# Optimization experiments

Measured on AMD Instinct MI355X. Metric: run time of the kernel, lower is better.

The kernel has to match this reference:

```python
import jax, jax.numpy as jnp
import numpy as np

N_NODES = 50000
N_EDGES = 500000
D_IN = 128
D_HID = 128
OUTPUT_DIM = 10.0


def gcn_conv(x, src, dst, edge_weight, W, b, n_nodes):
    # PyG GCNConv: out = D^{-1/2} (A + I) D^{-1/2} X W + b, self-loop weight 1
    xw = x @ W  # [N, D_out]
    # degree at target nodes, including self-loop weight 1
    deg = jax.ops.segment_sum(edge_weight, dst, num_segments=n_nodes) + 1.0
    dinv = jnp.where(deg > 0, jax.lax.rsqrt(deg), 0.0)  # [N]
    norm = dinv[src] * edge_weight * dinv[dst]  # [E]
    msgs = xw[src] * norm[:, None]  # [E, D_out] gathered+scaled messages
    agg = jax.ops.segment_sum(msgs, dst, num_segments=n_nodes)
    # analytic self-loop contribution: norm_ii = dinv_i * 1 * dinv_i
    agg = agg + xw * (dinv * dinv)[:, None]
    return agg + b


def setup_inputs() -> dict:
    key = jax.random.key(0)
    k = jax.random.split(key, 8)
    x = jax.random.normal(k[0], (N_NODES, D_IN), dtype=jnp.float32)
    edge_index = jax.random.randint(k[1], (2, N_EDGES), 0, N_NODES, dtype=jnp.int64)
    edge_weight = jax.random.uniform(k[2], (N_EDGES,), dtype=jnp.float32)
    s1 = 1.0 / np.sqrt(D_IN)
    s2 = 1.0 / np.sqrt(D_HID)
    W1 = jax.random.uniform(k[3], (D_IN, D_HID), minval=-s1, maxval=s1, dtype=jnp.float32)
    b1 = jnp.zeros((D_HID,), dtype=jnp.float32)
    W2 = jax.random.uniform(k[4], (D_HID, D_HID), minval=-s2, maxval=s2, dtype=jnp.float32)
    b2 = jnp.zeros((D_HID,), dtype=jnp.float32)
    Wf = jax.random.uniform(k[5], (D_HID, 1), minval=-s2, maxval=s2, dtype=jnp.float32)
    bf = jax.random.uniform(k[6], (1,), minval=-s2, maxval=s2, dtype=jnp.float32)
    return {"x": x, "edge_index": edge_index, "edge_weight": edge_weight,
            "W1": W1, "b1": b1, "W2": W2, "b2": b2, "Wf": Wf, "bf": bf}


def reference(x, edge_index, edge_weight, W1, b1, W2, b2, Wf, bf):
    src, dst = edge_index[0], edge_index[1]
    h = gcn_conv(x, src, dst, edge_weight, W1, b1, N_NODES)
    h = gcn_conv(h, src, dst, edge_weight, W2, b2, N_NODES)
    out = h @ Wf + bf  # [N, 1]
    return jax.nn.sigmoid(out) * OUTPUT_DIM
```

## Files before the change

kernel.cpp:

```cpp
#include <hip/hip_runtime.h>

#define N_NODES 50000
#define N_EDGES 500000
#define D 128
#define FXS 4194304.0f
#define CAP 64

typedef unsigned long long u64;

__global__ void pass1_kernel(const int* __restrict__ src, const int* __restrict__ dst,
                             const float* __restrict__ ew,
                             const float* __restrict__ W1, const float* __restrict__ W2,
                             const float* __restrict__ b1, const float* __restrict__ b2,
                             const float* __restrict__ Wf, const float* __restrict__ bf,
                             u64* __restrict__ degcnt, int2* __restrict__ pairs,
                             float* __restrict__ v, float* __restrict__ consts,
                             int eb) {
    if ((int)blockIdx.x == eb) {
        __shared__ float u[D];
        int t = threadIdx.x;
        if (t < D) {
            float a = 0.f;
#pragma unroll 8
            for (int j = 0; j < D; ++j) a += W2[t * D + j] * Wf[j];
            u[t] = a;
        }
        __syncthreads();
        if (t < D) {
            float a = 0.f;
#pragma unroll 8
            for (int k = 0; k < D; ++k) a += W1[t * D + k] * u[k];
            v[t] = a;
        }
        if (t == 0) {
            float c = 0.f;
            for (int k = 0; k < D; ++k) c += b1[k] * u[k];
            consts[0] = c;
        } else if (t == 1) {
            float c = bf[0];
            for (int k = 0; k < D; ++k) c += b2[k] * Wf[k];
            consts[1] = c;
        }
        return;
    }
    int tid = blockIdx.x * blockDim.x + threadIdx.x;
    if (tid < N_EDGES / 4) {
        int4   d = ((const int4*)dst)[tid];
        int4   s = ((const int4*)src)[tid];
        float4 w = ((const float4*)ew)[tid];
        unsigned f0 = __float2uint_rn(w.x * FXS);
        unsigned f1 = __float2uint_rn(w.y * FXS);
        unsigned f2 = __float2uint_rn(w.z * FXS);
        unsigned f3 = __float2uint_rn(w.w * FXS);
        u64 o0 = atomicAdd(&degcnt[d.x], (1ull << 32) | (u64)f0);
        u64 o1 = atomicAdd(&degcnt[d.y], (1ull << 32) | (u64)f1);
        u64 o2 = atomicAdd(&degcnt[d.z], (1ull << 32) | (u64)f2);
        u64 o3 = atomicAdd(&degcnt[d.w], (1ull << 32) | (u64)f3);
        int s0 = (int)(o0 >> 32), s1 = (int)(o1 >> 32);
        int s2 = (int)(o2 >> 32), s3 = (int)(o3 >> 32);
        if (s0 < CAP) pairs[d.x * CAP + s0] = make_int2(s.x, __float_as_int(w.x));
        if (s1 < CAP) pairs[d.y * CAP + s1] = make_int2(s.y, __float_as_int(w.y));
        if (s2 < CAP) pairs[d.z * CAP + s2] = make_int2(s.z, __float_as_int(w.z));
        if (s3 < CAP) pairs[d.w * CAP + s3] = make_int2(s.w, __float_as_int(w.w));
    }
}

__global__ void gemv_kernel(const float* __restrict__ x, const float* __restrict__ v,
                            const u64* __restrict__ degcnt,
                            float* __restrict__ dinv, float* __restrict__ tw,
                            int* __restrict__ cntv) {
    __shared__ float vs[D];
    const int t = threadIdx.x;
    if (t < D) vs[t] = v[t];
    __syncthreads();
    const int l = t & 31;
    const int n = blockIdx.x * 8 + (t >> 5);
    float4 xv = ((const float4*)(x + (size_t)n * D))[l];
    float a = xv.x * vs[l * 4] + xv.y * vs[l * 4 + 1] +
              xv.z * vs[l * 4 + 2] + xv.w * vs[l * 4 + 3];
#pragma unroll
    for (int off = 16; off > 0; off >>= 1) a += __shfl_xor(a, off);
    if (l == 0) {
        u64 dc = degcnt[n];
        int c = (int)(dc >> 32);
        float deg = (float)(unsigned)(dc & 0xffffffffu) * (1.0f / FXS);
        float di = rsqrtf(deg + 1.0f);
        dinv[n] = di;
        cntv[n] = (c < CAP) ? c : CAP;
        tw[n] = di * a;
    }
}

__global__ void gather_s_kernel(const float* __restrict__ tw, const float* __restrict__ dinv,
                                const int* __restrict__ cntv, const int2* __restrict__ pairs,
                                const float* __restrict__ consts, float* __restrict__ sw) {
    int tid = threadIdx.x;
    int n = blockIdx.x * 64 + (tid >> 2);
    int l = tid & 3;
    if (n >= N_NODES) return;
    int cnt = cntv[n];
    const int4* row = (const int4*)(pairs + (size_t)n * CAP);
    float acc = 0.f;
    for (int c = l; 2 * c < cnt; c += 4) {
        int4 p = row[c];
        acc += __int_as_float(p.y) * tw[p.x];
        if (2 * c + 1 < cnt) acc += __int_as_float(p.w) * tw[p.z];
    }
    acc += __shfl_xor(acc, 1);
    acc += __shfl_xor(acc, 2);
    if (l == 0) {
        float di = dinv[n];
        float s = di * (acc + tw[n]) + consts[0];
        sw[n] = di * s;
    }
}

__global__ void gather_z_kernel(const float* __restrict__ sw, const float* __restrict__ dinv,
                                const int* __restrict__ cntv, const int2* __restrict__ pairs,
                                const float* __restrict__ consts, float* __restrict__ out) {
    int tid = threadIdx.x;
    int n = blockIdx.x * 64 + (tid >> 2);
    int l = tid & 3;
    if (n >= N_NODES) return;
    int cnt = cntv[n];
    const int4* row = (const int4*)(pairs + (size_t)n * CAP);
    float acc = 0.f;
    for (int c = l; 2 * c < cnt; c += 4) {
        int4 p = row[c];
        acc += __int_as_float(p.y) * sw[p.x];
        if (2 * c + 1 < cnt) acc += __int_as_float(p.w) * sw[p.z];
    }
    acc += __shfl_xor(acc, 1);
    acc += __shfl_xor(acc, 2);
    if (l == 0) {
        float di = dinv[n];
        float z = di * (acc + sw[n]) + consts[1];
        out[n] = 10.0f / (1.0f + expf(-z));
    }
}

extern "C" void kernel_launch(void* const* d_in, const int* in_sizes, int n_in,
                              void* d_out, int out_size, void* d_ws, size_t ws_size,
                              hipStream_t stream) {
    const float* x  = (const float*)d_in[0];
    const int*   ei = (const int*)d_in[1];
    const float* ew = (const float*)d_in[2];
    const float* W1 = (const float*)d_in[3];
    const float* b1 = (const float*)d_in[4];
    const float* W2 = (const float*)d_in[5];
    const float* b2 = (const float*)d_in[6];
    const float* Wf = (const float*)d_in[7];
    const float* bf = (const float*)d_in[8];
    const int* srcv = ei;
    const int* dstv = ei + N_EDGES;
    float* out = (float*)d_out;

    char* p = (char*)d_ws;
    auto alloc = [&](size_t bytes) { void* r = (void*)p; p += (bytes + 255) & ~(size_t)255; return r; };
    u64*   degcnt = (u64*)alloc((size_t)N_NODES * 8);
    float* dinv   = (float*)alloc(N_NODES * 4);
    int*   cntv   = (int*)alloc(N_NODES * 4);
    float* tw     = (float*)alloc(N_NODES * 4);
    float* sw     = (float*)alloc(N_NODES * 4);
    float* v      = (float*)alloc(D * 4);
    float* consts = (float*)alloc(2 * 4);
    int2*  pairs  = (int2*)alloc((size_t)N_NODES * CAP * 8);

    const int EB = (N_EDGES / 4 + 255) / 256;
    const int GB = (N_NODES + 63) / 64;

    hipMemsetAsync(degcnt, 0, (size_t)N_NODES * 8, stream);

    pass1_kernel<<<EB + 1, 256, 0, stream>>>(srcv, dstv, ew, W1, W2, b1, b2, Wf, bf,
                                             degcnt, pairs, v, consts, EB);

    gemv_kernel<<<N_NODES / 8, 256, 0, stream>>>(x, v, degcnt, dinv, tw, cntv);

    gather_s_kernel<<<GB, 256, 0, stream>>>(tw, dinv, cntv, pairs, consts, sw);
    gather_z_kernel<<<GB, 256, 0, stream>>>(sw, dinv, cntv, pairs, consts, out);
}
```

Before: 131.2 us.

## Replace global 64-bit atomic bucketing with LDS chunk histograms, scan, and placement

Edge bucketing by destination moves off global 64-bit atomics. It now uses three phases. A per-chunk histogram is built in shared memory with 8-bit packed counters, a per-node scan over chunks produces base offsets, and a placement pass uses LDS atomics to assign slots. Degrees are computed in the gemv kernel by summing the stored edge weights rather than by fixed-point atomic accumulation. The aim is to remove contended global atomics and the memset, at the cost of extra kernels, a 256x50000-byte histogram round trip, and the risk of 8-bit counter overflow for high-degree nodes within a chunk. Degree now also ignores edges beyond CAP.

```diff
diff --git a/kernel.cpp b/kernel.cpp
--- a/kernel.cpp
+++ b/kernel.cpp
@@ -3,20 +3,20 @@
 #define N_NODES 50000
 #define N_EDGES 500000
 #define D 128
-#define FXS 4194304.0f
 #define CAP 64
+#define NCHUNK 256
+#define EPC ((N_EDGES + NCHUNK - 1) / NCHUNK)
+#define NWORDS ((N_NODES + 3) / 4)
 
 typedef unsigned long long u64;
 
-__global__ void pass1_kernel(const int* __restrict__ src, const int* __restrict__ dst,
-                             const float* __restrict__ ew,
-                             const float* __restrict__ W1, const float* __restrict__ W2,
-                             const float* __restrict__ b1, const float* __restrict__ b2,
-                             const float* __restrict__ Wf, const float* __restrict__ bf,
-                             u64* __restrict__ degcnt, int2* __restrict__ pairs,
-                             float* __restrict__ v, float* __restrict__ consts,
-                             int eb) {
-    if ((int)blockIdx.x == eb) {
+__global__ void hist_kernel(const int* __restrict__ dst,
+                            const float* __restrict__ W1, const float* __restrict__ W2,
+                            const float* __restrict__ b1, const float* __restrict__ b2,
+                            const float* __restrict__ Wf, const float* __restrict__ bf,
+                            unsigned* __restrict__ hist32, float* __restrict__ v,
+                            float* __restrict__ consts) {
+    if ((int)blockIdx.x == NCHUNK) {
         __shared__ float u[D];
         int t = threadIdx.x;
         if (t < D) {
@@ -43,32 +43,60 @@
         }
         return;
     }
-    int tid = blockIdx.x * blockDim.x + threadIdx.x;
-    if (tid < N_EDGES / 4) {
-        int4   d = ((const int4*)dst)[tid];
-        int4   s = ((const int4*)src)[tid];
-        float4 w = ((const float4*)ew)[tid];
-        unsigned f0 = __float2uint_rn(w.x * FXS);
-        unsigned f1 = __float2uint_rn(w.y * FXS);
-        unsigned f2 = __float2uint_rn(w.z * FXS);
-        unsigned f3 = __float2uint_rn(w.w * FXS);
-        u64 o0 = atomicAdd(&degcnt[d.x], (1ull << 32) | (u64)f0);
-        u64 o1 = atomicAdd(&degcnt[d.y], (1ull << 32) | (u64)f1);
-        u64 o2 = atomicAdd(&degcnt[d.z], (1ull << 32) | (u64)f2);
-        u64 o3 = atomicAdd(&degcnt[d.w], (1ull << 32) | (u64)f3);
-        int s0 = (int)(o0 >> 32), s1 = (int)(o1 >> 32);
-        int s2 = (int)(o2 >> 32), s3 = (int)(o3 >> 32);
-        if (s0 < CAP) pairs[d.x * CAP + s0] = make_int2(s.x, __float_as_int(w.x));
-        if (s1 < CAP) pairs[d.y * CAP + s1] = make_int2(s.y, __float_as_int(w.y));
-        if (s2 < CAP) pairs[d.z * CAP + s2] = make_int2(s.z, __float_as_int(w.z));
-        if (s3 < CAP) pairs[d.w * CAP + s3] = make_int2(s.w, __float_as_int(w.w));
+    __shared__ unsigned lds[NWORDS];
+    const int t = threadIdx.x;
+    const int c = blockIdx.x;
+    for (int i = t; i < NWORDS; i += 256) lds[i] = 0u;
+    __syncthreads();
+    const int e0 = c * EPC;
+    const int e1 = (e0 + EPC < N_EDGES) ? e0 + EPC : N_EDGES;
+    for (int e = e0 + t; e < e1; e += 256) {
+        int d = dst[e];
+        atomicAdd(&lds[d >> 2], 1u << (8 * (d & 3)));
+    }
+    __syncthreads();
+    unsigned* outw = hist32 + (size_t)c * NWORDS;
+    for (int i = t; i < NWORDS; i += 256) outw[i] = lds[i];
+}
+
+__global__ void scan_kernel(const unsigned char* __restrict__ hist8,
+                            unsigned char* __restrict__ base8, int* __restrict__ cntv) {
+    int n = blockIdx.x * blockDim.x + threadIdx.x;
+    if (n >= N_NODES) return;
+    int run = 0;
+#pragma unroll 8
+    for (int c = 0; c < NCHUNK; ++c) {
+        int b = hist8[(size_t)c * (NWORDS * 4) + n];
+        base8[(size_t)c * (NWORDS * 4) + n] = (unsigned char)run;
+        run += b;
+    }
+    cntv[n] = (run < CAP) ? run : CAP;
+}
+
+__global__ void place_kernel(const int* __restrict__ src, const int* __restrict__ dst,
+                             const float* __restrict__ ew,
+                             const unsigned* __restrict__ base32, int2* __restrict__ pairs) {
+    __shared__ unsigned lds[NWORDS];
+    const int t = threadIdx.x;
+    const int c = blockIdx.x;
+    const unsigned* inw = base32 + (size_t)c * NWORDS;
+    for (int i = t; i < NWORDS; i += 256) lds[i] = inw[i];
+    __syncthreads();
+    const int e0 = c * EPC;
+    const int e1 = (e0 + EPC < N_EDGES) ? e0 + EPC : N_EDGES;
+    for (int e = e0 + t; e < e1; e += 256) {
+        int d = dst[e];
+        int sh = 8 * (d & 3);
+        unsigned old = atomicAdd(&lds[d >> 2], 1u << sh);
+        int slot = (int)((old >> sh) & 0xffu);
+        if (slot < CAP)
+            pairs[(size_t)d * CAP + slot] = make_int2(src[e], __float_as_int(ew[e]));
     }
 }
 
 __global__ void gemv_kernel(const float* __restrict__ x, const float* __restrict__ v,
-                            const u64* __restrict__ degcnt,
-                            float* __restrict__ dinv, float* __restrict__ tw,
-                            int* __restrict__ cntv) {
+                            const int2* __restrict__ pairs, const int* __restrict__ cntv,
+                            float* __restrict__ dinv, float* __restrict__ tw) {
     __shared__ float vs[D];
     const int t = threadIdx.x;
     if (t < D) vs[t] = v[t];
@@ -78,15 +106,18 @@
     float4 xv = ((const float4*)(x + (size_t)n * D))[l];
     float a = xv.x * vs[l * 4] + xv.y * vs[l * 4 + 1] +
               xv.z * vs[l * 4 + 2] + xv.w * vs[l * 4 + 3];
+    int cnt = cntv[n];
+    const int2* row = pairs + (size_t)n * CAP;
+    float wsum = 0.f;
+    for (int i = l; i < cnt; i += 32) wsum += __int_as_float(row[i].y);
 #pragma unroll
-    for (int off = 16; off > 0; off >>= 1) a += __shfl_xor(a, off);
+    for (int off = 16; off > 0; off >>= 1) {
+        a    += __shfl_xor(a, off);
+        wsum += __shfl_xor(wsum, off);
+    }
     if (l == 0) {
-        u64 dc = degcnt[n];
-        int c = (int)(dc >> 32);
-        float deg = (float)(unsigned)(dc & 0xffffffffu) * (1.0f / FXS);
-        float di = rsqrtf(deg + 1.0f);
+        float di = rsqrtf(wsum + 1.0f);
         dinv[n] = di;
-        cntv[n] = (c < CAP) ? c : CAP;
         tw[n] = di * a;
     }
 }
@@ -157,24 +188,28 @@
 
     char* p = (char*)d_ws;
     auto alloc = [&](size_t bytes) { void* r = (void*)p; p += (bytes + 255) & ~(size_t)255; return r; };
-    u64*   degcnt = (u64*)alloc((size_t)N_NODES * 8);
+    unsigned*      hist32 = (unsigned*)alloc((size_t)NCHUNK * NWORDS * 4);
+    unsigned char* base8  = (unsigned char*)alloc((size_t)NCHUNK * NWORDS * 4);
+    int*   cntv   = (int*)alloc(N_NODES * 4);
     float* dinv   = (float*)alloc(N_NODES * 4);
-    int*   cntv   = (int*)alloc(N_NODES * 4);
     float* tw     = (float*)alloc(N_NODES * 4);
     float* sw     = (float*)alloc(N_NODES * 4);
     float* v      = (float*)alloc(D * 4);
     float* consts = (float*)alloc(2 * 4);
     int2*  pairs  = (int2*)alloc((size_t)N_NODES * CAP * 8);
 
-    const int EB = (N_EDGES / 4 + 255) / 256;
     const int GB = (N_NODES + 63) / 64;
-
-    hipMemsetAsync(degcnt, 0, (size_t)N_NODES * 8, stream);
-
-    pass1_kernel<<<EB + 1, 256, 0, stream>>>(srcv, dstv, ew, W1, W2, b1, b2, Wf, bf,
-                                             degcnt, pairs, v, consts, EB);
-
-    gemv_kernel<<<N_NODES / 8, 256, 0, stream>>>(x, v, degcnt, dinv, tw, cntv);
+    const int NB = (N_NODES + 255) / 256;
+
+    hist_kernel<<<NCHUNK + 1, 256, 0, stream>>>(dstv, W1, W2, b1, b2, Wf, bf,
+                                                hist32, v, consts);
+
+    scan_kernel<<<NB, 256, 0, stream>>>((const unsigned char*)hist32, base8, cntv);
+
+    place_kernel<<<NCHUNK, 256, 0, stream>>>(srcv, dstv, ew,
+                                             (const unsigned*)base8, pairs);
+
+    gemv_kernel<<<N_NODES / 8, 256, 0, stream>>>(x, v, pairs, cntv, dinv, tw);
 
     gather_s_kernel<<<GB, 256, 0, stream>>>(tw, dinv, cntv, pairs, consts, sw);
     gather_z_kernel<<<GB, 256, 0, stream>>>(sw, dinv, cntv, pairs, consts, out);
```

Result: slower. 140.8 us (+7.4%).

## Overlap edge scatter with node GEMV in one kernel, pad degree atomics

Applied to the files above, without the earlier changes.

The weight-folding prep and the degree-array zeroing move into one prep kernel, which replaces the memset. The edge atomic/scatter pass and the x·v GEMV now run as disjoint block ranges of a single work kernel, so the two can execute at the same time. The per-node finalize becomes a small epilogue kernel. Degree counters are padded to 64 bytes per node to spread atomic contention across cache lines, at the cost of an 8x larger zeroing pass and an extra intermediate array.

```diff
diff --git a/kernel.cpp b/kernel.cpp
--- a/kernel.cpp
+++ b/kernel.cpp
@@ -5,20 +5,20 @@
 #define D 128
 #define FXS 4194304.0f
 #define CAP 64
+#define DPAD 8
+#define EBLK 489
+#define GEMVB 2048
 
 typedef unsigned long long u64;
 
-__global__ void pass1_kernel(const int* __restrict__ src, const int* __restrict__ dst,
-                             const float* __restrict__ ew,
-                             const float* __restrict__ W1, const float* __restrict__ W2,
-                             const float* __restrict__ b1, const float* __restrict__ b2,
-                             const float* __restrict__ Wf, const float* __restrict__ bf,
-                             u64* __restrict__ degcnt, int2* __restrict__ pairs,
-                             float* __restrict__ v, float* __restrict__ consts,
-                             int eb) {
-    if ((int)blockIdx.x == eb) {
+__global__ void prep_kernel(const float* __restrict__ W1, const float* __restrict__ W2,
+                            const float* __restrict__ b1, const float* __restrict__ b2,
+                            const float* __restrict__ Wf, const float* __restrict__ bf,
+                            float* __restrict__ v, float* __restrict__ consts,
+                            u64* __restrict__ degcnt) {
+    const int t = threadIdx.x;
+    if (blockIdx.x == 0) {
         __shared__ float u[D];
-        int t = threadIdx.x;
         if (t < D) {
             float a = 0.f;
 #pragma unroll 8
@@ -43,51 +43,68 @@
         }
         return;
     }
-    int tid = blockIdx.x * blockDim.x + threadIdx.x;
-    if (tid < N_EDGES / 4) {
-        int4   d = ((const int4*)dst)[tid];
-        int4   s = ((const int4*)src)[tid];
-        float4 w = ((const float4*)ew)[tid];
-        unsigned f0 = __float2uint_rn(w.x * FXS);
-        unsigned f1 = __float2uint_rn(w.y * FXS);
-        unsigned f2 = __float2uint_rn(w.z * FXS);
-        unsigned f3 = __float2uint_rn(w.w * FXS);
-        u64 o0 = atomicAdd(&degcnt[d.x], (1ull << 32) | (u64)f0);
-        u64 o1 = atomicAdd(&degcnt[d.y], (1ull << 32) | (u64)f1);
-        u64 o2 = atomicAdd(&degcnt[d.z], (1ull << 32) | (u64)f2);
-        u64 o3 = atomicAdd(&degcnt[d.w], (1ull << 32) | (u64)f3);
-        int s0 = (int)(o0 >> 32), s1 = (int)(o1 >> 32);
-        int s2 = (int)(o2 >> 32), s3 = (int)(o3 >> 32);
-        if (s0 < CAP) pairs[d.x * CAP + s0] = make_int2(s.x, __float_as_int(w.x));
-        if (s1 < CAP) pairs[d.y * CAP + s1] = make_int2(s.y, __float_as_int(w.y));
-        if (s2 < CAP) pairs[d.z * CAP + s2] = make_int2(s.z, __float_as_int(w.z));
-        if (s3 < CAP) pairs[d.w * CAP + s3] = make_int2(s.w, __float_as_int(w.w));
+    for (int i = (blockIdx.x - 1) * 256 + t; i < N_NODES * DPAD; i += 255 * 256)
+        degcnt[i] = 0ull;
+}
+
+__global__ void work_kernel(const int* __restrict__ src, const int* __restrict__ dst,
+                            const float* __restrict__ ew, const float* __restrict__ x,
+                            const float* __restrict__ v,
+                            u64* __restrict__ degcnt, int2* __restrict__ pairs,
+                            float* __restrict__ traw) {
+    const int t = threadIdx.x;
+    const int bid = blockIdx.x;
+    if (bid < EBLK) {
+        int q = bid * 256 + t;
+        if (q < N_EDGES / 4) {
+            int4   d4 = ((const int4*)dst)[q];
+            int4   s4 = ((const int4*)src)[q];
+            float4 w4 = ((const float4*)ew)[q];
+            unsigned f0 = __float2uint_rn(w4.x * FXS);
+            unsigned f1 = __float2uint_rn(w4.y * FXS);
+            unsigned f2 = __float2uint_rn(w4.z * FXS);
+            unsigned f3 = __float2uint_rn(w4.w * FXS);
+            u64 o0 = atomicAdd(&degcnt[(size_t)d4.x * DPAD], (1ull << 32) | (u64)f0);
+            u64 o1 = atomicAdd(&degcnt[(size_t)d4.y * DPAD], (1ull << 32) | (u64)f1);
+            u64 o2 = atomicAdd(&degcnt[(size_t)d4.z * DPAD], (1ull << 32) | (u64)f2);
+            u64 o3 = atomicAdd(&degcnt[(size_t)d4.w * DPAD], (1ull << 32) | (u64)f3);
+            int s0 = (int)(o0 >> 32), s1 = (int)(o1 >> 32);
+            int s2 = (int)(o2 >> 32), s3 = (int)(o3 >> 32);
+            if (s0 < CAP) pairs[(size_t)d4.x * CAP + s0] = make_int2(s4.x, __float_as_int(w4.x));
+            if (s1 < CAP) pairs[(size_t)d4.y * CAP + s1] = make_int2(s4.y, __float_as_int(w4.y));
+            if (s2 < CAP) pairs[(size_t)d4.z * CAP + s2] = make_int2(s4.z, __float_as_int(w4.z));
+            if (s3 < CAP) pairs[(size_t)d4.w * CAP + s3] = make_int2(s4.w, __float_as_int(w4.w));
+        }
+        return;
+    }
+    __shared__ float vs[D];
+    if (t < D) vs[t] = v[t];
+    __syncthreads();
+    const int l = t & 31;
+    const int sub = t >> 5;
+    for (int g = bid - EBLK; g < N_NODES / 8; g += GEMVB) {
+        int n = g * 8 + sub;
+        float4 xv = ((const float4*)(x + (size_t)n * D))[l];
+        float a = xv.x * vs[l * 4] + xv.y * vs[l * 4 + 1] +
+                  xv.z * vs[l * 4 + 2] + xv.w * vs[l * 4 + 3];
+#pragma unroll
+        for (int off = 16; off > 0; off >>= 1) a += __shfl_xor(a, off);
+        if (l == 0) traw[n] = a;
     }
 }
 
-__global__ void gemv_kernel(const float* __restrict__ x, const float* __restrict__ v,
-                            const u64* __restrict__ degcnt,
-                            float* __restrict__ dinv, float* __restrict__ tw,
-                            int* __restrict__ cntv) {
-    __shared__ float vs[D];
-    const int t = threadIdx.x;
-    if (t < D) vs[t] = v[t];
-    __syncthreads();
-    const int l = t & 31;
-    const int n = blockIdx.x * 8 + (t >> 5);
-    float4 xv = ((const float4*)(x + (size_t)n * D))[l];
-    float a = xv.x * vs[l * 4] + xv.y * vs[l * 4 + 1] +
-              xv.z * vs[l * 4 + 2] + xv.w * vs[l * 4 + 3];
-#pragma unroll
-    for (int off = 16; off > 0; off >>= 1) a += __shfl_xor(a, off);
-    if (l == 0) {
-        u64 dc = degcnt[n];
+__global__ void epi_kernel(const u64* __restrict__ degcnt, const float* __restrict__ traw,
+                           float* __restrict__ dinv, int* __restrict__ cntv,
+                           float* __restrict__ tw) {
+    int n = blockIdx.x * blockDim.x + threadIdx.x;
+    if (n < N_NODES) {
+        u64 dc = degcnt[(size_t)n * DPAD];
         int c = (int)(dc >> 32);
         float deg = (float)(unsigned)(dc & 0xffffffffu) * (1.0f / FXS);
         float di = rsqrtf(deg + 1.0f);
         dinv[n] = di;
         cntv[n] = (c < CAP) ? c : CAP;
-        tw[n] = di * a;
+        tw[n] = di * traw[n];
     }
 }
 
@@ -157,24 +174,25 @@
 
     char* p = (char*)d_ws;
     auto alloc = [&](size_t bytes) { void* r = (void*)p; p += (bytes + 255) & ~(size_t)255; return r; };
-    u64*   degcnt = (u64*)alloc((size_t)N_NODES * 8);
+    u64*   degcnt = (u64*)alloc((size_t)N_NODES * DPAD * 8);
     float* dinv   = (float*)alloc(N_NODES * 4);
     int*   cntv   = (int*)alloc(N_NODES * 4);
+    float* traw   = (float*)alloc(N_NODES * 4);
     float* tw     = (float*)alloc(N_NODES * 4);
     float* sw     = (float*)alloc(N_NODES * 4);
     float* v      = (float*)alloc(D * 4);
     float* consts = (float*)alloc(2 * 4);
     int2*  pairs  = (int2*)alloc((size_t)N_NODES * CAP * 8);
 
-    const int EB = (N_EDGES / 4 + 255) / 256;
     const int GB = (N_NODES + 63) / 64;
+    const int NB = (N_NODES + 255) / 256;
 
-    hipMemsetAsync(degcnt, 0, (size_t)N_NODES * 8, stream);
+    prep_kernel<<<256, 256, 0, stream>>>(W1, W2, b1, b2, Wf, bf, v, consts, degcnt);
 
-    pass1_kernel<<<EB + 1, 256, 0, stream>>>(srcv, dstv, ew, W1, W2, b1, b2, Wf, bf,
-                                             degcnt, pairs, v, consts, EB);
+    work_kernel<<<EBLK + GEMVB, 256, 0, stream>>>(srcv, dstv, ew, x, v,
+                                                  degcnt, pairs, traw);
 
-    gemv_kernel<<<N_NODES / 8, 256, 0, stream>>>(x, v, degcnt, dinv, tw, cntv);
+    epi_kernel<<<NB, 256, 0, stream>>>(degcnt, traw, dinv, cntv, tw);
 
     gather_s_kernel<<<GB, 256, 0, stream>>>(tw, dinv, cntv, pairs, consts, sw);
     gather_z_kernel<<<GB, 256, 0, stream>>>(sw, dinv, cntv, pairs, consts, out);
```

New measurement: 139.0 us. 1.06x slower.
